# Kernel tuning notes

Measured on AMD Instinct MI355X. Metric: run time of the kernel, lower is better.

The kernel has to match this reference:

```python
import jax, jax.numpy as jnp
import numpy as np

FI_BIT, FI_GROUP = 8, 64
FW_BIT, FW_GROUP = 8, 64


def quantize_bfp(x, bit, group):
    """Block-floating-point quantize: groups of `group` elems along the last dim
    share the exponent of the group max; mantissas are rounded to `bit` bits."""
    shp = x.shape
    xg = x.reshape(shp[:-1] + (shp[-1] // group, group))
    maxabs = jnp.max(jnp.abs(xg), axis=-1, keepdims=True)
    e = jnp.floor(jnp.log2(jnp.maximum(maxabs, jnp.asarray(1e-38, x.dtype))))
    step = jnp.exp2(e - (bit - 1))  # quantization step for shared exponent e
    qmax = 2 ** (bit - 1) - 1
    q = jnp.clip(jnp.round(xg / step), -(qmax + 1), qmax) * step
    q = jnp.where(maxabs == 0, jnp.zeros_like(q), q)
    return q.reshape(shp)


def setup_inputs() -> dict:
    key = jax.random.key(0)
    k1, k2, k3 = jax.random.split(key, 3)
    N, IN, OUT = 4096, 4096, 4096
    x = jax.random.normal(k1, (N, IN), dtype=jnp.float32)
    # weight/bias initialized uniform(-0.1, 0.1) as in the torch module
    weight = jax.random.uniform(k2, (OUT, IN), dtype=jnp.float32, minval=-0.1, maxval=0.1)
    bias = jax.random.uniform(k3, (OUT,), dtype=jnp.float32, minval=-0.1, maxval=0.1)
    return {"x": x, "weight": weight, "bias": bias}


def reference(x, weight, bias):
    xq = quantize_bfp(x, FI_BIT, FI_GROUP)          # [N, IN]
    wq = quantize_bfp(weight, FW_BIT, FW_GROUP)     # [OUT, IN]
    out = jnp.einsum('ni,oi->no', xq, wq)
    # Faithful to the original forward: F.linear adds bias once, then the
    # explicit `output += bias` adds it a second time.
    out = out + 2.0 * bias[None, :]
    return out
```

## Files before the change

kernel.cpp:

```cpp
#include <hip/hip_runtime.h>
#include <stdint.h>

typedef __bf16 bf16_t;
typedef __attribute__((ext_vector_type(8))) __bf16 bf16x8;
typedef __attribute__((ext_vector_type(4))) float f32x4;

#define NDIM 4096

__global__ __launch_bounds__(256) void quant_bfp(const float* __restrict__ in0,
                                                 bf16_t* __restrict__ out0,
                                                 const float* __restrict__ in1,
                                                 bf16_t* __restrict__ out1) {
    const float* in = blockIdx.y ? in1 : in0;
    bf16_t* out     = blockIdx.y ? out1 : out0;
    const int stride = gridDim.x * 256;
    for (int t = blockIdx.x * 256 + threadIdx.x; t < NDIM * NDIM / 4; t += stride) {
        float4 v = ((const float4*)in)[t];
        float m = fmaxf(fmaxf(fabsf(v.x), fabsf(v.y)), fmaxf(fabsf(v.z), fabsf(v.w)));
        m = fmaxf(m, __shfl_xor(m, 1));
        m = fmaxf(m, __shfl_xor(m, 2));
        m = fmaxf(m, __shfl_xor(m, 4));
        m = fmaxf(m, __shfl_xor(m, 8));
        const int e = (int)((__float_as_uint(m) >> 23) & 0xFF) - 127;
        float step = __uint_as_float((uint32_t)(e + 120) << 23);
        float inv  = __uint_as_float((uint32_t)(134 - e) << 23);
        if (m == 0.0f) { step = 0.0f; inv = 0.0f; }
        float q0 = fminf(fmaxf(rintf(v.x * inv), -128.0f), 127.0f) * step;
        float q1 = fminf(fmaxf(rintf(v.y * inv), -128.0f), 127.0f) * step;
        float q2 = fminf(fmaxf(rintf(v.z * inv), -128.0f), 127.0f) * step;
        float q3 = fminf(fmaxf(rintf(v.w * inv), -128.0f), 127.0f) * step;
        union { bf16_t b[4]; uint2 u; } o;
        o.b[0] = (bf16_t)q0; o.b[1] = (bf16_t)q1;
        o.b[2] = (bf16_t)q2; o.b[3] = (bf16_t)q3;
        ((uint2*)out)[t] = o.u;
    }
}

__device__ __forceinline__ void g2l16(const bf16_t* g, void* l) {
    __builtin_amdgcn_global_load_lds(
        (__attribute__((address_space(1))) void*)g,
        (__attribute__((address_space(3))) void*)l, 16, 0, 0);
}

#define FENCE() asm volatile("" ::: "memory")
#define BAR()   do { FENCE(); __builtin_amdgcn_sched_barrier(0);              \
                     __builtin_amdgcn_s_barrier();                            \
                     __builtin_amdgcn_sched_barrier(0); FENCE(); } while (0)
#define WAITV(n) asm volatile("s_waitcnt vmcnt(" #n ")" ::: "memory")

#define STAGE_A(b, r, ko) do {                                                  \
    g2l16(gA + (size_t)((r) * 64) * NDIM + (ko),                                \
          (char*)sA + (b) * 32768 + (r) * 16384 + tid * 16);                    \
    g2l16(gA + (size_t)((r) * 64 + 128) * NDIM + (ko),                          \
          (char*)sA + (b) * 32768 + (r) * 16384 + 8192 + tid * 16);             \
} while (0)
#define STAGE_B(b, r, ko) do {                                                  \
    g2l16(gB + (size_t)((r) * 32) * NDIM + (ko),                                \
          (char*)sB + (b) * 32768 + (r) * 16384 + tid * 16);                    \
    g2l16(gB + (size_t)((r) * 32 + 128) * NDIM + (ko),                          \
          (char*)sB + (b) * 32768 + (r) * 16384 + 8192 + tid * 16);             \
} while (0)

#define LDA(b, qm) do {                                                         \
    _Pragma("unroll")                                                           \
    for (int i_ = 0; i_ < 4; ++i_) {                                            \
        const int r_ = (b) * 16384 + (qm) * 8192 + aRow + i_ * 1024;            \
        afr[i_][0] = *(const bf16x8*)&sA[r_ + ce0];                             \
        afr[i_][1] = *(const bf16x8*)&sA[r_ + ce1];                             \
    }                                                                           \
} while (0)
#define LDB(b, qn) do {                                                         \
    _Pragma("unroll")                                                           \
    for (int j_ = 0; j_ < 2; ++j_) {                                            \
        const int r_ = (b) * 16384 + (qn) * 8192 + bRow + j_ * 1024;            \
        bfr[qn][j_][0] = *(const bf16x8*)&sB[r_ + ce0];                         \
        bfr[qn][j_][1] = *(const bf16x8*)&sB[r_ + ce1];                         \
    }                                                                           \
} while (0)

#define MFMAQ(qm, qn) do {                                                      \
    __builtin_amdgcn_s_setprio(1);                                              \
    _Pragma("unroll")                                                           \
    for (int i_ = 0; i_ < 4; ++i_)                                              \
        _Pragma("unroll")                                                       \
        for (int j_ = 0; j_ < 2; ++j_) {                                        \
            acc[(qm)*4+i_][(qn)*2+j_] = __builtin_amdgcn_mfma_f32_16x16x32_bf16(\
                afr[i_][0], bfr[qn][j_][0], acc[(qm)*4+i_][(qn)*2+j_], 0, 0, 0);\
            acc[(qm)*4+i_][(qn)*2+j_] = __builtin_amdgcn_mfma_f32_16x16x32_bf16(\
                afr[i_][1], bfr[qn][j_][1], acc[(qm)*4+i_][(qn)*2+j_], 0, 0, 0);\
        }                                                                       \
    __builtin_amdgcn_s_setprio(0);                                              \
} while (0)

__global__ __launch_bounds__(512, 2) void gemm_bfp(const bf16_t* __restrict__ A,
                                                   const bf16_t* __restrict__ B,
                                                   const float* __restrict__ bias,
                                                   float* __restrict__ C) {
    __shared__ bf16_t sA[2 * 256 * 64];
    __shared__ bf16_t sB[2 * 256 * 64];

    const int tid  = threadIdx.x;
    const int wave = tid >> 6;
    const int lane = tid & 63;
    const int wr   = wave >> 2;
    const int wc   = wave & 3;

    const int p  = blockIdx.x;
    const int wg = (p & 7) * 32 + (p >> 3);
    const int bm = wg >> 4;
    const int bn = wg & 15;

    const int srow = tid >> 3;
    const int swz  = ((tid & 7) ^ (srow & 7)) * 8;
    const bf16_t* gA = A + (size_t)(bm * 256 + srow) * NDIM + swz;
    const bf16_t* gB = B + (size_t)(bn * 256 + (srow >> 5) * 64 + (srow & 31)) * NDIM + swz;

    const int quad = lane >> 4;
    const int l16  = lane & 15;
    const int rsw  = l16 & 7;
    const int ce0  = (quad ^ rsw) * 8;
    const int ce1  = ((4 + quad) ^ rsw) * 8;
    const int aRow = (wr * 64 + l16) * 64;
    const int bRow = (wc * 32 + l16) * 64;

    f32x4 acc[8][4];
#pragma unroll
    for (int i = 0; i < 8; ++i)
#pragma unroll
        for (int j = 0; j < 4; ++j) acc[i][j] = (f32x4){0.0f, 0.0f, 0.0f, 0.0f};

    bf16x8 afr[4][2];
    bf16x8 bfr[2][2][2];

    STAGE_A(0, 0, 0); STAGE_B(0, 0, 0); STAGE_B(0, 1, 0); STAGE_A(0, 1, 0);
    STAGE_A(1, 0, 64); STAGE_B(1, 0, 64); STAGE_B(1, 1, 64);
    WAITV(6);

    for (int kt = 0; kt < NDIM; kt += 128) {
        const int koA1 = kt + 64;
        const int koN2 = (kt + 128 < NDIM) ? kt + 128 : 0;
        const int koB3 = (kt + 192 < NDIM) ? kt + 192 : 0;

        BAR();
        LDA(0, 0); LDB(0, 0);
        STAGE_A(1, 1, koA1);
        MFMAQ(0, 0);

        BAR();
        LDB(0, 1);
        STAGE_A(0, 0, koN2);
        MFMAQ(0, 1);

        BAR();
        LDA(0, 1);
        STAGE_B(0, 0, koN2);
        MFMAQ(1, 1);

        BAR();
        STAGE_B(0, 1, koN2);
        MFMAQ(1, 0);
        WAITV(6);

        BAR();
        LDA(1, 0); LDB(1, 0);
        STAGE_A(0, 1, koN2);
        MFMAQ(0, 0);

        BAR();
        LDB(1, 1);
        STAGE_A(1, 0, koB3);
        MFMAQ(0, 1);

        BAR();
        LDA(1, 1);
        STAGE_B(1, 0, koB3);
        MFMAQ(1, 1);

        BAR();
        STAGE_B(1, 1, koB3);
        MFMAQ(1, 0);
        WAITV(6);
    }

    const int row0 = bm * 256 + wr * 128 + quad * 4;
    const int col0 = bn * 256 + wc * 64 + l16;
#pragma unroll
    for (int nj = 0; nj < 4; ++nj) {
        const int c = col0 + nj * 16;
        const float bv = 2.0f * bias[c];
#pragma unroll
        for (int mi = 0; mi < 8; ++mi) {
            const int r = row0 + mi * 16;
#pragma unroll
            for (int reg = 0; reg < 4; ++reg)
                C[(size_t)(r + reg) * NDIM + c] = acc[mi][nj][reg] + bv;
        }
    }
}

extern "C" void kernel_launch(void* const* d_in, const int* in_sizes, int n_in,
                              void* d_out, int out_size, void* d_ws, size_t ws_size,
                              hipStream_t stream) {
    const float* x    = (const float*)d_in[0];
    const float* w    = (const float*)d_in[1];
    const float* bias = (const float*)d_in[2];
    float* out = (float*)d_out;

    bf16_t* xq = (bf16_t*)d_ws;
    bf16_t* wq = xq + (size_t)NDIM * NDIM;

    dim3 qgrid(1024, 2);
    quant_bfp<<<qgrid, 256, 0, stream>>>(x, xq, w, wq);

    dim3 grid(256);
    gemm_bfp<<<grid, 512, 0, stream>>>(xq, wq, bias, out);
}
```

Measured before the change: 284.4 us.

## Shrink GEMM tile to 256x128 with register double-buffered fragment pipeline

Result: slower. 320.9 us (+12.8%).

```diff
diff --git a/kernel.cpp b/kernel.cpp
--- a/kernel.cpp
+++ b/kernel.cpp
@@ -47,47 +47,44 @@
                      __builtin_amdgcn_s_barrier();                            \
                      __builtin_amdgcn_sched_barrier(0); FENCE(); } while (0)
 #define WAITV(n) asm volatile("s_waitcnt vmcnt(" #n ")" ::: "memory")
+#define LGKM0()  asm volatile("s_waitcnt lgkmcnt(0)" ::: "memory")
 
-#define STAGE_A(b, r, ko) do {                                                  \
-    g2l16(gA + (size_t)((r) * 64) * NDIM + (ko),                                \
-          (char*)sA + (b) * 32768 + (r) * 16384 + tid * 16);                    \
-    g2l16(gA + (size_t)((r) * 64 + 128) * NDIM + (ko),                          \
-          (char*)sA + (b) * 32768 + (r) * 16384 + 8192 + tid * 16);             \
-} while (0)
-#define STAGE_B(b, r, ko) do {                                                  \
-    g2l16(gB + (size_t)((r) * 32) * NDIM + (ko),                                \
-          (char*)sB + (b) * 32768 + (r) * 16384 + tid * 16);                    \
-    g2l16(gB + (size_t)((r) * 32 + 128) * NDIM + (ko),                          \
-          (char*)sB + (b) * 32768 + (r) * 16384 + 8192 + tid * 16);             \
+#define STAGE(bf, koff) do {                                                    \
+    _Pragma("unroll")                                                           \
+    for (int i_ = 0; i_ < 4; ++i_)                                              \
+        g2l16(gA + (size_t)(i_ * 64) * NDIM + (koff),                           \
+              (char*)sA + (bf) * 32768 + i_ * 8192 + tid * 16);                 \
+    _Pragma("unroll")                                                           \
+    for (int j_ = 0; j_ < 2; ++j_)                                              \
+        g2l16(gB + (size_t)(j_ * 64) * NDIM + (koff),                           \
+              (char*)sB + (bf) * 16384 + j_ * 8192 + tid * 16);                 \
 } while (0)
 
-#define LDA(b, qm) do {                                                         \
+#define READS(fa, fb, bf) do {                                                  \
     _Pragma("unroll")                                                           \
     for (int i_ = 0; i_ < 4; ++i_) {                                            \
-        const int r_ = (b) * 16384 + (qm) * 8192 + aRow + i_ * 1024;            \
-        afr[i_][0] = *(const bf16x8*)&sA[r_ + ce0];                             \
-        afr[i_][1] = *(const bf16x8*)&sA[r_ + ce1];                             \
+        const int r_ = (bf) * 16384 + aRow + i_ * 1024;                         \
+        fa[i_][0] = *(const bf16x8*)&sA[r_ + ce0];                              \
+        fa[i_][1] = *(const bf16x8*)&sA[r_ + ce1];                              \
     }                                                                           \
-} while (0)
-#define LDB(b, qn) do {                                                         \
     _Pragma("unroll")                                                           \
-    for (int j_ = 0; j_ < 2; ++j_) {                                            \
-        const int r_ = (b) * 16384 + (qn) * 8192 + bRow + j_ * 1024;            \
-        bfr[qn][j_][0] = *(const bf16x8*)&sB[r_ + ce0];                         \
-        bfr[qn][j_][1] = *(const bf16x8*)&sB[r_ + ce1];                         \
+    for (int j_ = 0; j_ < 4; ++j_) {                                            \
+        const int r_ = (bf) * 8192 + bRow + j_ * 1024;                          \
+        fb[j_][0] = *(const bf16x8*)&sB[r_ + ce0];                              \
+        fb[j_][1] = *(const bf16x8*)&sB[r_ + ce1];                              \
     }                                                                           \
 } while (0)
 
-#define MFMAQ(qm, qn) do {                                                      \
+#define MFMAT(fa, fb) do {                                                      \
     __builtin_amdgcn_s_setprio(1);                                              \
     _Pragma("unroll")                                                           \
     for (int i_ = 0; i_ < 4; ++i_)                                              \
         _Pragma("unroll")                                                       \
-        for (int j_ = 0; j_ < 2; ++j_) {                                        \
-            acc[(qm)*4+i_][(qn)*2+j_] = __builtin_amdgcn_mfma_f32_16x16x32_bf16(\
-                afr[i_][0], bfr[qn][j_][0], acc[(qm)*4+i_][(qn)*2+j_], 0, 0, 0);\
-            acc[(qm)*4+i_][(qn)*2+j_] = __builtin_amdgcn_mfma_f32_16x16x32_bf16(\
-                afr[i_][1], bfr[qn][j_][1], acc[(qm)*4+i_][(qn)*2+j_], 0, 0, 0);\
+        for (int j_ = 0; j_ < 4; ++j_) {                                        \
+            acc[i_][j_] = __builtin_amdgcn_mfma_f32_16x16x32_bf16(              \
+                fa[i_][0], fb[j_][0], acc[i_][j_], 0, 0, 0);                    \
+            acc[i_][j_] = __builtin_amdgcn_mfma_f32_16x16x32_bf16(              \
+                fa[i_][1], fb[j_][1], acc[i_][j_], 0, 0, 0);                    \
         }                                                                       \
     __builtin_amdgcn_s_setprio(0);                                              \
 } while (0)
@@ -97,99 +94,76 @@
                                                    const float* __restrict__ bias,
                                                    float* __restrict__ C) {
     __shared__ bf16_t sA[2 * 256 * 64];
-    __shared__ bf16_t sB[2 * 256 * 64];
+    __shared__ bf16_t sB[2 * 128 * 64];
 
     const int tid  = threadIdx.x;
     const int wave = tid >> 6;
     const int lane = tid & 63;
-    const int wr   = wave >> 2;
-    const int wc   = wave & 3;
+    const int wm   = wave >> 1;
+    const int wn   = wave & 1;
 
     const int p  = blockIdx.x;
-    const int wg = (p & 7) * 32 + (p >> 3);
-    const int bm = wg >> 4;
-    const int bn = wg & 15;
+    const int wg = (p & 7) * 64 + (p >> 3);
+    const int bm = wg >> 5;
+    const int bn = wg & 31;
 
     const int srow = tid >> 3;
     const int swz  = ((tid & 7) ^ (srow & 7)) * 8;
     const bf16_t* gA = A + (size_t)(bm * 256 + srow) * NDIM + swz;
-    const bf16_t* gB = B + (size_t)(bn * 256 + (srow >> 5) * 64 + (srow & 31)) * NDIM + swz;
+    const bf16_t* gB = B + (size_t)(bn * 128 + srow) * NDIM + swz;
 
     const int quad = lane >> 4;
     const int l16  = lane & 15;
     const int rsw  = l16 & 7;
     const int ce0  = (quad ^ rsw) * 8;
     const int ce1  = ((4 + quad) ^ rsw) * 8;
-    const int aRow = (wr * 64 + l16) * 64;
-    const int bRow = (wc * 32 + l16) * 64;
+    const int aRow = (wm * 64 + l16) * 64;
+    const int bRow = (wn * 64 + l16) * 64;
 
-    f32x4 acc[8][4];
+    f32x4 acc[4][4];
 #pragma unroll
-    for (int i = 0; i < 8; ++i)
+    for (int i = 0; i < 4; ++i)
 #pragma unroll
         for (int j = 0; j < 4; ++j) acc[i][j] = (f32x4){0.0f, 0.0f, 0.0f, 0.0f};
 
-    bf16x8 afr[4][2];
-    bf16x8 bfr[2][2][2];
+    bf16x8 fAe[4][2], fBe[4][2];
+    bf16x8 fAo[4][2], fBo[4][2];
 
-    STAGE_A(0, 0, 0); STAGE_B(0, 0, 0); STAGE_B(0, 1, 0); STAGE_A(0, 1, 0);
-    STAGE_A(1, 0, 64); STAGE_B(1, 0, 64); STAGE_B(1, 1, 64);
+    STAGE(0, 0);
+    STAGE(1, 64);
     WAITV(6);
+    BAR();
+    READS(fAe, fBe, 0);
 
-    for (int kt = 0; kt < NDIM; kt += 128) {
-        const int koA1 = kt + 64;
-        const int koN2 = (kt + 128 < NDIM) ? kt + 128 : 0;
-        const int koB3 = (kt + 192 < NDIM) ? kt + 192 : 0;
+    for (int t = 0; t < 64; t += 2) {
+        const int k2 = (t + 2 < 64) ? (t + 2) * 64 : 0;
+        const int k3 = (t + 3 < 64) ? (t + 3) * 64 : 0;
 
+        LGKM0();
         BAR();
-        LDA(0, 0); LDB(0, 0);
-        STAGE_A(1, 1, koA1);
-        MFMAQ(0, 0);
+        STAGE(0, k2);
+        WAITV(6);
+        BAR();
+        READS(fAo, fBo, 1);
+        MFMAT(fAe, fBe);
 
+        LGKM0();
         BAR();
-        LDB(0, 1);
-        STAGE_A(0, 0, koN2);
-        MFMAQ(0, 1);
-
+        STAGE(1, k3);
+        WAITV(6);
         BAR();
-        LDA(0, 1);
-        STAGE_B(0, 0, koN2);
-        MFMAQ(1, 1);
-
-        BAR();
-        STAGE_B(0, 1, koN2);
-        MFMAQ(1, 0);
-        WAITV(6);
-
-        BAR();
-        LDA(1, 0); LDB(1, 0);
-        STAGE_A(0, 1, koN2);
-        MFMAQ(0, 0);
-
-        BAR();
-        LDB(1, 1);
-        STAGE_A(1, 0, koB3);
-        MFMAQ(0, 1);
-
-        BAR();
-        LDA(1, 1);
-        STAGE_B(1, 0, koB3);
-        MFMAQ(1, 1);
-
-        BAR();
-        STAGE_B(1, 1, koB3);
-        MFMAQ(1, 0);
-        WAITV(6);
+        READS(fAe, fBe, 0);
+        MFMAT(fAo, fBo);
     }
 
-    const int row0 = bm * 256 + wr * 128 + quad * 4;
-    const int col0 = bn * 256 + wc * 64 + l16;
+    const int row0 = bm * 256 + wm * 64 + quad * 4;
+    const int col0 = bn * 128 + wn * 64 + l16;
 #pragma unroll
     for (int nj = 0; nj < 4; ++nj) {
         const int c = col0 + nj * 16;
         const float bv = 2.0f * bias[c];
 #pragma unroll
-        for (int mi = 0; mi < 8; ++mi) {
+        for (int mi = 0; mi < 4; ++mi) {
             const int r = row0 + mi * 16;
 #pragma unroll
             for (int reg = 0; reg < 4; ++reg)
@@ -212,6 +186,6 @@
     dim3 qgrid(1024, 2);
     quant_bfp<<<qgrid, 256, 0, stream>>>(x, xq, w, wq);
 
-    dim3 grid(256);
+    dim3 grid(512);
     gemm_bfp<<<grid, 512, 0, stream>>>(xq, wq, bias, out);
 }
```
